# Kernel tuning notes

Measured on AMD Instinct MI355X. Metric: run time of the kernel, lower is better.

Reference implementation:

```python
import jax, jax.numpy as jnp
import numpy as np

BN_EPS = 1e-5


def _conv(x, w, stride, pad):
    return jax.lax.conv_general_dilated(
        x, w, (stride, stride), [(pad, pad), (pad, pad)],
        dimension_numbers=('NCHW', 'OIHW', 'NCHW'))


def setup_inputs() -> dict:
    key = jax.random.key(0)
    ks = jax.random.split(key, 6)
    b, c, h, w = 8, 32, 80, 160
    guidance = jax.random.normal(ks[0], (b, c, 2 * h, 2 * w), dtype=jnp.float32)
    # positive disparities, realistic magnitude
    disp = jax.random.uniform(ks[1], (b, 1, h, w), dtype=jnp.float32) * 24.0
    conv1_w = jax.random.normal(ks[2], (2 * c, c, 3, 3), dtype=jnp.float32) * 0.05
    bn_gamma = jnp.ones((2 * c,), dtype=jnp.float32)
    bn_beta = jnp.zeros((2 * c,), dtype=jnp.float32)
    bn_mean = jax.random.normal(ks[3], (2 * c,), dtype=jnp.float32) * 0.1
    bn_var = jax.random.uniform(ks[4], (2 * c,), dtype=jnp.float32, minval=0.5, maxval=1.5)
    conv2_w = jax.random.normal(ks[5], (9 * 64, 2 * c, 3, 3), dtype=jnp.float32) * 0.05
    return {'guidance': guidance, 'disp': disp, 'conv1_w': conv1_w,
            'bn_gamma': bn_gamma, 'bn_beta': bn_beta, 'bn_mean': bn_mean,
            'bn_var': bn_var, 'conv2_w': conv2_w}


def reference(guidance, disp, conv1_w, bn_gamma, bn_beta, bn_mean, bn_var, conv2_w):
    b, _, h, w = disp.shape
    # mask branch: convbn(stride 2) + ReLU + conv -> 9*64 channels at (h, w)
    x = _conv(guidance, conv1_w, 2, 1)
    inv = jax.lax.rsqrt(bn_var + BN_EPS)
    x = (x - bn_mean[None, :, None, None]) * (inv * bn_gamma)[None, :, None, None] + bn_beta[None, :, None, None]
    x = jax.nn.relu(x)
    mask = _conv(x, conv2_w, 1, 1).reshape(b, 1, 9, 8, 8, h, w)
    mask = jax.nn.softmax(mask, axis=2)
    # unfold(8*disp, 3x3, pad=1) -> (b, 1, 9, h, w), row-major kernel order
    d8 = jnp.pad(8.0 * disp, ((0, 0), (0, 0), (1, 1), (1, 1)))
    patches = jnp.stack([d8[:, :, i:i + h, j:j + w]
                         for i in range(3) for j in range(3)], axis=2)
    # convex combination over the 9 neighbors
    up = jnp.sum(mask * patches[:, :, :, None, None], axis=2)  # (b,1,8,8,h,w)
    up = up.transpose(0, 1, 4, 2, 5, 3)  # (b,1,h,8,w,8)
    return up.reshape(b, 1, 8 * h, 8 * w)
```

## Files before the change

### kernel.cpp

```cpp
#include <hip/hip_runtime.h>
#include <math.h>

typedef _Float16 half8 __attribute__((ext_vector_type(8)));
typedef float f32x4 __attribute__((ext_vector_type(4)));

constexpr int B_ = 8;
constexpr int HG = 160, WG = 320;
constexpr int H = 80, W = 160;
constexpr size_t CWS_OFF  = 0;
constexpr size_t W1WS_OFF = 663552;
constexpr size_t XG_OFF   = 700416;

__global__ __launch_bounds__(256) void prep(const float* __restrict__ w1,
                                            const float* __restrict__ w2,
                                            char* __restrict__ ws)
{
    int e = blockIdx.x * 256 + threadIdx.x;
    if (e < 576 * 64) {
        int n = e >> 6, cin = e & 63;
        int k = n >> 6, ng = (n >> 4) & 3, nl = n & 15;
        int kl = cin & 31, c5 = cin >> 5;
        const float* src = w2 + ((size_t)(n * 64 + cin)) * 9;
        int fragoff = ((kl >> 3) * 16 + nl) * 16 + (kl & 7) * 2;
#pragma unroll
        for (int t = 0; t < 9; ++t) {
            int s = t * 2 + c5;
            *(_Float16*)(ws + CWS_OFF + (size_t)ng * 165888
                         + (size_t)(s * 9 + k) * 1024 + fragoff) = (_Float16)src[t];
        }
    } else if (e < 576 * 64 + 64 * 32) {
        int e2 = e - 576 * 64;
        int ch = e2 >> 5, cin = e2 & 31;
        const float* src = w1 + ((size_t)(ch * 32 + cin)) * 9;
        int fragoff = (ch >> 4) * 1024 + ((cin >> 3) * 16 + (ch & 15)) * 16 + (cin & 7) * 2;
#pragma unroll
        for (int t = 0; t < 9; ++t)
            *(_Float16*)(ws + W1WS_OFF + (size_t)t * 4096 + fragoff) = (_Float16)src[t];
    }
}

__global__ __launch_bounds__(256, 4) void conv1_mfma(
    const float* __restrict__ g, const char* __restrict__ ws_w1,
    const float* __restrict__ gamma, const float* __restrict__ beta,
    const float* __restrict__ mean, const float* __restrict__ var,
    _Float16* __restrict__ xg)
{
    const int tx0 = blockIdx.x * 16, ty0 = blockIdx.y * 8, b = blockIdx.z;
    __shared__ __align__(16) _Float16 gl[2][17][18][32];
    const int tid = threadIdx.x;

    const int gy0 = 2 * ty0 - 1;
    const int gxa0 = 2 * tx0 - 2;
    for (int i = tid; i < 17 * 32 * 17; i += 256) {
        int wr = i / 544; int rem = i - wr * 544;
        int cin = rem / 17; int c2 = rem - cin * 17;
        int gy = gy0 + wr;
        int gxa = gxa0 + 2 * c2;
        float2 v = make_float2(0.f, 0.f);
        if (gy >= 0 && gy < HG && gxa >= 0)
            v = *(const float2*)(g + ((size_t)(b * 32 + cin) * HG + gy) * WG + gxa);
        int slot = cin >> 3, elem = cin & 7;
        if (c2 > 0) {
            int wch = c2 - 1;
            gl[1][wr][wch][((slot ^ ((wch >> 1) & 3)) << 3) + elem] = (_Float16)v.x;
        }
        {
            int wch = c2;
            gl[0][wr][wch][((slot ^ ((wch >> 1) & 3)) << 3) + elem] = (_Float16)v.y;
        }
    }

    const int lane = tid & 63, w = tid >> 6;
    const int c = lane & 15, grp = lane >> 4;

    const _Float16* w1p = (const _Float16*)ws_w1 + lane * 8;
    half8 bf[4];
#pragma unroll
    for (int nt = 0; nt < 4; ++nt) bf[nt] = *(const half8*)(w1p + nt * 512);

    f32x4 zf = {0.f, 0.f, 0.f, 0.f};
    f32x4 acc[2][4];
#pragma unroll
    for (int mt = 0; mt < 2; ++mt)
#pragma unroll
        for (int nt = 0; nt < 4; ++nt) acc[mt][nt] = zf;

    __syncthreads();

#pragma unroll
    for (int s = 0; s < 9; ++s) {
        const int dy = s / 3, dx = s - dy * 3;
        const int par = dx & 1, dxh = dx >> 1;
        half8 af[2];
#pragma unroll
        for (int mt = 0; mt < 2; ++mt) {
            int wr = 2 * (2 * w + mt) + dy;
            int wch = c + dxh;
            af[mt] = *(const half8*)&gl[par][wr][wch][(grp ^ ((wch >> 1) & 3)) << 3];
        }
        const _Float16* wnext = w1p + (size_t)(s + 1) * 2048;
#pragma unroll
        for (int nt = 0; nt < 4; ++nt) {
            half8 cur = bf[nt];
            bf[nt] = *(const half8*)(wnext + nt * 512);
            acc[0][nt] = __builtin_amdgcn_mfma_f32_16x16x32_f16(af[0], cur, acc[0][nt], 0, 0, 0);
            acc[1][nt] = __builtin_amdgcn_mfma_f32_16x16x32_f16(af[1], cur, acc[1][nt], 0, 0, 0);
        }
    }

#pragma unroll
    for (int nt = 0; nt < 4; ++nt) {
        int ch = nt * 16 + c;
        float mu = mean[ch], scv = rsqrtf(var[ch] + 1e-5f) * gamma[ch], bt = beta[ch];
#pragma unroll
        for (int mt = 0; mt < 2; ++mt) {
            int y = ty0 + 2 * w + mt;
#pragma unroll
            for (int r = 0; r < 4; ++r) {
                int x = tx0 + grp * 4 + r;
                float v = fmaxf((acc[mt][nt][r] - mu) * scv + bt, 0.f);
                xg[(((size_t)(b * H + y) * W + x) << 6) + ch] = (_Float16)v;
            }
        }
    }
}

__global__ __launch_bounds__(256, 2) void conv2_mfma(
    const _Float16* __restrict__ xg, const char* __restrict__ ws_c,
    const float* __restrict__ disp, float* __restrict__ out)
{
    const int tx0 = blockIdx.x * 16, ty0 = blockIdx.y * 4, b = blockIdx.z;
    __shared__ __align__(16) _Float16 xs[108 * 64];
    __shared__ float d8s[108];
    const int tid = threadIdx.x;
    const int lane = tid & 63, wid = tid >> 6;
    const int c = lane & 15, grp = lane >> 4;

    half8 zero8;
#pragma unroll
    for (int j = 0; j < 8; ++j) zero8[j] = (_Float16)0.f;
    for (int cidx = tid; cidx < 864; cidx += 256) {
        int wpx = cidx >> 3, slot = cidx & 7;
        int rr = wpx / 18, cc = wpx - rr * 18;
        int y = ty0 - 1 + rr, xc = tx0 - 1 + cc;
        half8 v = zero8;
        if (y >= 0 && y < H && xc >= 0 && xc < W)
            v = *(const half8*)(xg + (((size_t)(b * H + y) * W + xc) << 6) + slot * 8);
        *(half8*)&xs[wpx * 64 + (slot ^ (wpx & 7)) * 8] = v;
    }
    if (tid < 108) {
        int rr = tid / 18, cc = tid - rr * 18;
        int y = ty0 - 1 + rr, xc = tx0 - 1 + cc;
        float v = 0.f;
        if (y >= 0 && y < H && xc >= 0 && xc < W) v = 8.f * disp[(b * H + y) * W + xc];
        d8s[tid] = v;
    }

    f32x4 zf = {0.f, 0.f, 0.f, 0.f};
    f32x4 acc[4][9];
#pragma unroll
    for (int m = 0; m < 4; ++m)
#pragma unroll
        for (int k = 0; k < 9; ++k) acc[m][k] = zf;

    const _Float16* wp = (const _Float16*)ws_c + (size_t)wid * 82944 + lane * 8;

    const int lb = (blockIdx.z * 20 + blockIdx.y) * 10 + blockIdx.x;
    const int s0 = (lb * 7) % 18;

    half8 bf[9];
#pragma unroll
    for (int k = 0; k < 9; ++k) bf[k] = *(const half8*)(wp + (size_t)s0 * 4608 + k * 512);

    __syncthreads();

    int s = s0;
#pragma unroll 2
    for (int i = 0; i < 18; ++i) {
        int sn = s + 1; if (sn == 18) sn = 0;
        const int t = s >> 1;
        const int dy = t / 3, dx = t - dy * 3;
        const int aslot = (s & 1) * 4 + grp;
        half8 af[4];
#pragma unroll
        for (int mt = 0; mt < 4; ++mt) {
            int wrow = (mt + dy) * 18 + c + dx;
            af[mt] = *(const half8*)&xs[wrow * 64 + (aslot ^ (wrow & 7)) * 8];
        }
        const _Float16* wnext = wp + (size_t)sn * 4608;
#pragma unroll
        for (int k = 0; k < 9; ++k) {
            half8 cur = bf[k];
            bf[k] = *(const half8*)(wnext + k * 512);
#pragma unroll
            for (int mt = 0; mt < 4; ++mt)
                acc[mt][k] = __builtin_amdgcn_mfma_f32_16x16x32_f16(
                    af[mt], cur, acc[mt][k], 0, 0, 0);
        }
        s = sn;
    }

    const int ij = wid * 16 + c;
    const int oi = ij >> 3, oj = ij & 7;
#pragma unroll
    for (int mt = 0; mt < 4; ++mt) {
#pragma unroll
        for (int r = 0; r < 4; ++r) {
            int pr = mt, pc = grp * 4 + r;
            float pat[9];
#pragma unroll
            for (int k9 = 0; k9 < 9; ++k9) pat[k9] = d8s[(pr + k9 / 3) * 18 + pc + k9 % 3];
            float mx = acc[mt][0][r];
#pragma unroll
            for (int k9 = 1; k9 < 9; ++k9) mx = fmaxf(mx, acc[mt][k9][r]);
            float sum = 0.f, up = 0.f;
#pragma unroll
            for (int k9 = 0; k9 < 9; ++k9) {
                float e = __expf(acc[mt][k9][r] - mx);
                sum += e; up += e * pat[k9];
            }
            int y = ty0 + pr, xc = tx0 + pc;
            out[((size_t)(b * (8 * H) + y * 8 + oi)) * (size_t)(8 * W) + xc * 8 + oj] = up / sum;
        }
    }
}

extern "C" void kernel_launch(void* const* d_in, const int* in_sizes, int n_in,
                              void* d_out, int out_size, void* d_ws, size_t ws_size,
                              hipStream_t stream)
{
    const float* guidance = (const float*)d_in[0];
    const float* disp     = (const float*)d_in[1];
    const float* conv1_w  = (const float*)d_in[2];
    const float* bn_gamma = (const float*)d_in[3];
    const float* bn_beta  = (const float*)d_in[4];
    const float* bn_mean  = (const float*)d_in[5];
    const float* bn_var   = (const float*)d_in[6];
    const float* conv2_w  = (const float*)d_in[7];
    float* out = (float*)d_out;
    char* ws = (char*)d_ws;
    _Float16* xg = (_Float16*)(ws + XG_OFF);

    prep<<<dim3((576 * 64 + 64 * 32 + 255) / 256), dim3(256), 0, stream>>>(
        conv1_w, conv2_w, ws);
    dim3 grid1(W / 16, H / 8, B_);
    conv1_mfma<<<grid1, dim3(256), 0, stream>>>(
        guidance, ws + W1WS_OFF, bn_gamma, bn_beta, bn_mean, bn_var, xg);
    dim3 grid2(W / 16, H / 4, B_);
    conv2_mfma<<<grid2, dim3(256), 0, stream>>>(
        xg, ws + CWS_OFF, disp, out);
}
```

Before: 110.8 us.

## Split conv2 softmax neighbors across wave pairs with online-softmax merge

Each conv2 block now handles half of the output subpixel groups. Its four waves split the 9 softmax neighbors 5/4, and each wave keeps only 5 or 4 accumulator sets instead of 9. The partial max, sum and weighted sum are merged through shared memory using a log-sum-exp combine. This lowers register pressure so occupancy can rise to three blocks per SIMD pair, and it doubles the grid. The cost is that the activation tile is loaded twice, and the change adds a synchronization plus extra shared memory.

```diff
diff --git a/kernel.cpp b/kernel.cpp
--- a/kernel.cpp
+++ b/kernel.cpp
@@ -125,16 +125,130 @@
     }
 }
 
-__global__ __launch_bounds__(256, 2) void conv2_mfma(
+template<int KB, int NK>
+__device__ __forceinline__ void conv2_half(
+    const _Float16* __restrict__ wp, const _Float16* __restrict__ xs,
+    const float* __restrict__ d8s, float (*part)[4][16][16][4],
+    int c, int grp, int ngl, int ng, int s0, int b, int tx0, int ty0,
+    float* __restrict__ out)
+{
+    f32x4 zf = {0.f, 0.f, 0.f, 0.f};
+    f32x4 acc[4][NK];
+#pragma unroll
+    for (int m = 0; m < 4; ++m)
+#pragma unroll
+        for (int f = 0; f < NK; ++f) acc[m][f] = zf;
+
+    half8 bf[NK];
+#pragma unroll
+    for (int f = 0; f < NK; ++f)
+        bf[f] = *(const half8*)(wp + (size_t)s0 * 4608 + (KB + f) * 512);
+
+    int s = s0;
+#pragma unroll 2
+    for (int i = 0; i < 18; ++i) {
+        int sn = s + 1; if (sn == 18) sn = 0;
+        const int t = s >> 1;
+        const int dy = t / 3, dx = t - dy * 3;
+        const int aslot = (s & 1) * 4 + grp;
+        half8 af[4];
+#pragma unroll
+        for (int mt = 0; mt < 4; ++mt) {
+            int wrow = (mt + dy) * 18 + c + dx;
+            af[mt] = *(const half8*)&xs[wrow * 64 + (aslot ^ (wrow & 7)) * 8];
+        }
+        const _Float16* wnext = wp + (size_t)sn * 4608;
+#pragma unroll
+        for (int f = 0; f < NK; ++f) {
+            half8 cur = bf[f];
+            bf[f] = *(const half8*)(wnext + (KB + f) * 512);
+#pragma unroll
+            for (int mt = 0; mt < 4; ++mt)
+                acc[mt][f] = __builtin_amdgcn_mfma_f32_16x16x32_f16(
+                    af[mt], cur, acc[mt][f], 0, 0, 0);
+        }
+        s = sn;
+    }
+
+    if (KB != 0) {
+#pragma unroll
+        for (int mt = 0; mt < 4; ++mt) {
+#pragma unroll
+            for (int r = 0; r < 4; ++r) {
+                const int pc = grp * 4 + r;
+                float m = acc[mt][0][r];
+#pragma unroll
+                for (int f = 1; f < NK; ++f) m = fmaxf(m, acc[mt][f][r]);
+                float S = 0.f, U = 0.f;
+#pragma unroll
+                for (int f = 0; f < NK; ++f) {
+                    const int k = KB + f;
+                    float e = __expf(acc[mt][f][r] - m);
+                    S += e;
+                    U += e * d8s[(mt + k / 3) * 18 + pc + k % 3];
+                }
+                float4 pv = make_float4(m, S, U, 0.f);
+                *(float4*)&part[ngl][mt][pc][c][0] = pv;
+            }
+        }
+        __syncthreads();
+    } else {
+        float pm[4][4], pS[4][4], pU[4][4];
+#pragma unroll
+        for (int mt = 0; mt < 4; ++mt) {
+#pragma unroll
+            for (int r = 0; r < 4; ++r) {
+                const int pc = grp * 4 + r;
+                float m = acc[mt][0][r];
+#pragma unroll
+                for (int f = 1; f < NK; ++f) m = fmaxf(m, acc[mt][f][r]);
+                float S = 0.f, U = 0.f;
+#pragma unroll
+                for (int f = 0; f < NK; ++f) {
+                    const int k = KB + f;
+                    float e = __expf(acc[mt][f][r] - m);
+                    S += e;
+                    U += e * d8s[(mt + k / 3) * 18 + pc + k % 3];
+                }
+                pm[mt][r] = m; pS[mt][r] = S; pU[mt][r] = U;
+            }
+        }
+        __syncthreads();
+        const int ij = ng * 16 + c;
+        const int oi = ij >> 3, oj = ij & 7;
+#pragma unroll
+        for (int mt = 0; mt < 4; ++mt) {
+#pragma unroll
+            for (int r = 0; r < 4; ++r) {
+                const int pc = grp * 4 + r;
+                float4 pv = *(const float4*)&part[ngl][mt][pc][c][0];
+                float mt_ = fmaxf(pm[mt][r], pv.x);
+                float e0 = __expf(pm[mt][r] - mt_);
+                float e1 = __expf(pv.x - mt_);
+                float sum = pS[mt][r] * e0 + pv.y * e1;
+                float up  = pU[mt][r] * e0 + pv.z * e1;
+                int y = ty0 + mt, xc = tx0 + pc;
+                out[((size_t)(b * (8 * H) + y * 8 + oi)) * (size_t)(8 * W)
+                    + xc * 8 + oj] = up / sum;
+            }
+        }
+    }
+}
+
+__global__ __launch_bounds__(256, 3) void conv2_mfma(
     const _Float16* __restrict__ xg, const char* __restrict__ ws_c,
     const float* __restrict__ disp, float* __restrict__ out)
 {
-    const int tx0 = blockIdx.x * 16, ty0 = blockIdx.y * 4, b = blockIdx.z;
+    const int h = blockIdx.x & 1;
+    const int tx0 = (blockIdx.x >> 1) * 16, ty0 = blockIdx.y * 4, b = blockIdx.z;
     __shared__ __align__(16) _Float16 xs[108 * 64];
     __shared__ float d8s[108];
+    __shared__ __align__(16) float part[2][4][16][16][4];
     const int tid = threadIdx.x;
     const int lane = tid & 63, wid = tid >> 6;
     const int c = lane & 15, grp = lane >> 4;
+    const int ngl = wid & 1, kh = wid >> 1;
+    const int ng = h * 2 + ngl;
 
     half8 zero8;
 #pragma unroll
@@ -156,73 +270,17 @@
         d8s[tid] = v;
     }
 
-    f32x4 zf = {0.f, 0.f, 0.f, 0.f};
-    f32x4 acc[4][9];
-#pragma unroll
-    for (int m = 0; m < 4; ++m)
-#pragma unroll
-        for (int k = 0; k < 9; ++k) acc[m][k] = zf;
-
-    const _Float16* wp = (const _Float16*)ws_c + (size_t)wid * 82944 + lane * 8;
-
-    const int lb = (blockIdx.z * 20 + blockIdx.y) * 10 + blockIdx.x;
+    const int lb = (blockIdx.z * 20 + blockIdx.y) * 20 + blockIdx.x;
     const int s0 = (lb * 7) % 18;
 
-    half8 bf[9];
-#pragma unroll
-    for (int k = 0; k < 9; ++k) bf[k] = *(const half8*)(wp + (size_t)s0 * 4608 + k * 512);
+    const _Float16* wp = (const _Float16*)ws_c + (size_t)ng * 82944 + lane * 8;
 
     __syncthreads();
 
-    int s = s0;
-#pragma unroll 2
-    for (int i = 0; i < 18; ++i) {
-        int sn = s + 1; if (sn == 18) sn = 0;
-        const int t = s >> 1;
-        const int dy = t / 3, dx = t - dy * 3;
-        const int aslot = (s & 1) * 4 + grp;
-        half8 af[4];
-#pragma unroll
-        for (int mt = 0; mt < 4; ++mt) {
-            int wrow = (mt + dy) * 18 + c + dx;
-            af[mt] = *(const half8*)&xs[wrow * 64 + (aslot ^ (wrow & 7)) * 8];
-        }
-        const _Float16* wnext = wp + (size_t)sn * 4608;
-#pragma unroll
-        for (int k = 0; k < 9; ++k) {
-            half8 cur = bf[k];
-            bf[k] = *(const half8*)(wnext + k * 512);
-#pragma unroll
-            for (int mt = 0; mt < 4; ++mt)
-                acc[mt][k] = __builtin_amdgcn_mfma_f32_16x16x32_f16(
-                    af[mt], cur, acc[mt][k], 0, 0, 0);
-        }
-        s = sn;
-    }
-
-    const int ij = wid * 16 + c;
-    const int oi = ij >> 3, oj = ij & 7;
-#pragma unroll
-    for (int mt = 0; mt < 4; ++mt) {
-#pragma unroll
-        for (int r = 0; r < 4; ++r) {
-            int pr = mt, pc = grp * 4 + r;
-            float pat[9];
-#pragma unroll
-            for (int k9 = 0; k9 < 9; ++k9) pat[k9] = d8s[(pr + k9 / 3) * 18 + pc + k9 % 3];
-            float mx = acc[mt][0][r];
-#pragma unroll
-            for (int k9 = 1; k9 < 9; ++k9) mx = fmaxf(mx, acc[mt][k9][r]);
-            float sum = 0.f, up = 0.f;
-#pragma unroll
-            for (int k9 = 0; k9 < 9; ++k9) {
-                float e = __expf(acc[mt][k9][r] - mx);
-                sum += e; up += e * pat[k9];
-            }
-            int y = ty0 + pr, xc = tx0 + pc;
-            out[((size_t)(b * (8 * H) + y * 8 + oi)) * (size_t)(8 * W) + xc * 8 + oj] = up / sum;
-        }
-    }
+    if (kh == 0)
+        conv2_half<0, 5>(wp, xs, d8s, part, c, grp, ngl, ng, s0, b, tx0, ty0, out);
+    else
+        conv2_half<5, 4>(wp, xs, d8s, part, c, grp, ngl, ng, s0, b, tx0, ty0, out);
 }
 
 extern "C" void kernel_launch(void* const* d_in, const int* in_sizes, int n_in,
@@ -246,7 +304,7 @@
     dim3 grid1(W / 16, H / 8, B_);
     conv1_mfma<<<grid1, dim3(256), 0, stream>>>(
         guidance, ws + W1WS_OFF, bn_gamma, bn_beta, bn_mean, bn_var, xg);
-    dim3 grid2(W / 16, H / 4, B_);
+    dim3 grid2(2 * W / 16, H / 4, B_);
     conv2_mfma<<<grid2, dim3(256), 0, stream>>>(
         xg, ws + CWS_OFF, disp, out);
 }
```

Result: slower. 119.8 us (+8.1%).
